# Performance work log

Measured on AMD Instinct MI355X. Metric: run time of the kernel, lower is better.

## Reference

```python
import jax, jax.numpy as jnp
import numpy as np

B, L, C = 2048, 2048, 16
F = L // 2                 # num_freqs = 1024
H = 4 * F                  # multi_factor * num_freqs = 4096
P = int(len(np.unique(L // np.arange(1, F + 1))))  # n patch sizes = 88
SCALE = 0.02
NOISE_EPS = 0.01


def setup_inputs() -> dict:
    key = jax.random.key(0)
    ks = jax.random.split(key, 10)
    return {
        "x": jax.random.normal(ks[0], (B, L, C), jnp.float32),
        "w_start": SCALE * jax.random.normal(ks[1], (C, 1), jnp.float32),
        "b_start": SCALE * jax.random.normal(ks[2], (1,), jnp.float32),
        "w1": SCALE * jax.random.normal(ks[3], (2, F, H), jnp.float32),
        "b1": SCALE * jax.random.normal(ks[4], (2, H), jnp.float32),
        "w2": SCALE * jax.random.normal(ks[5], (2, H, F), jnp.float32),
        "b2": SCALE * jax.random.normal(ks[6], (2, F), jnp.float32),
        "w_gate": SCALE * jax.random.normal(ks[7], (F, P), jnp.float32),
        "w_noise": SCALE * jax.random.normal(ks[8], (F, P), jnp.float32),
        "noise_z": jax.random.normal(ks[9], (B, P), jnp.float32),
        "top_k": 3,
    }


def reference(x, w_start, b_start, w1, b1, w2, b2, w_gate, w_noise, noise_z, top_k):
    # start_fc: [B, L, C] -> [B, L, 1] -> [B, 1, L]
    v = (jnp.einsum("blc,co->blo", x, w_start) + b_start).transpose(0, 2, 1)
    # rfft (ortho), drop DC bin -> [B, 1, F] complex
    xf = jnp.fft.rfft(v, axis=-1, norm="ortho")[:, :, 1:]
    xr, xi = jnp.real(xf), jnp.imag(xf)
    # complex 2-layer MLP in frequency domain
    o1r = jax.nn.relu(jnp.einsum("bdi,io->bdo", xr, w1[0]) - jnp.einsum("bdi,io->bdo", xi, w1[1]) + b1[0])
    o1i = jax.nn.relu(jnp.einsum("bdi,io->bdo", xi, w1[0]) + jnp.einsum("bdi,io->bdo", xr, w1[1]) + b1[1])
    o2r = jnp.einsum("bdo,of->bdf", o1r, w2[0]) - jnp.einsum("bdo,of->bdf", o1i, w2[1]) + b2[0]
    o2i = jnp.einsum("bdo,of->bdf", o1i, w2[0]) + jnp.einsum("bdo,of->bdf", o1r, w2[1]) + b2[1]
    amp = jnp.sqrt(o2r * o2r + o2i * o2i)[:, 0, :]  # [B, F]
    # router logits with (training) noise injection
    clean_logits = amp @ w_gate                      # [B, P]
    noise_std = jax.nn.softplus(amp @ w_noise) + NOISE_EPS
    logits = clean_logits + noise_z * noise_std
    # top-k -> softmax over top-k -> scatter into sparse gates
    top_w, top_i = jax.lax.top_k(logits, top_k)
    top_w = jax.nn.softmax(top_w, axis=-1)
    rows = jnp.arange(logits.shape[0])[:, None]
    gates = jnp.zeros_like(logits).at[rows, top_i].set(top_w)
    return gates
```

## Files before the change

kernel.cpp:

```cpp
#include <hip/hip_runtime.h>
#include <hip/hip_bf16.h>
#include <math.h>

#define B_DIM 2048
#define L_DIM 2048
#define F_DIM 1024
#define H_DIM 4096
#define P_DIM 88

typedef unsigned short u16;
typedef short bf16x8 __attribute__((ext_vector_type(8)));
typedef float f32x4 __attribute__((ext_vector_type(4)));

__device__ __forceinline__ u16 f2bf(float x) {
    unsigned u = __float_as_uint(x);
    return (u16)((u + 0x7fffu + ((u >> 16) & 1u)) >> 16);
}
__device__ __forceinline__ float bf2f(u16 h) {
    return __uint_as_float(((unsigned)h) << 16);
}

__device__ __forceinline__ void gload_lds16(const void* g, void* l) {
    unsigned loff = (unsigned)(uintptr_t)l;
    __builtin_amdgcn_global_load_lds(
        reinterpret_cast<const __attribute__((address_space(1))) void*>(
            reinterpret_cast<uintptr_t>(g)),
        reinterpret_cast<__attribute__((address_space(3))) void*>(loff),
        16, 0, 0);
}

__global__ __launch_bounds__(256) void prep_kernel(
    const float* __restrict__ x, const float* __restrict__ w_start,
    const float* __restrict__ b_start, u16* __restrict__ A1,
    const float* __restrict__ w1, u16* __restrict__ BT1)
{
    __shared__ float re[2048];
    __shared__ float im[2048];
    __shared__ float twr[1024];
    __shared__ float twi[1024];
    __shared__ float t0s[32][33];
    __shared__ float t1s[32][33];

    const int tid = threadIdx.x;

    if (blockIdx.x < 1024) {
        int b = blockIdx.x;
        const size_t row0 = (size_t)(2 * b) * 2048;

        const float4* wp = (const float4*)w_start;
        float4 w0 = wp[0], w1v = wp[1], w2 = wp[2], w3 = wp[3];
        float bs = b_start[0];

        for (int i = tid; i < 1024; i += 256) {
            float ang = -6.283185307179586f * ((float)i / 2048.0f);
            sincosf(ang, &twi[i], &twr[i]);
        }

        for (int l = tid; l < 2048; l += 256) {
            const float4* xp0 = (const float4*)(x + (row0 + l) * 16);
            const float4* xp1 = (const float4*)(x + (row0 + 2048 + l) * 16);
            float4 a0 = xp0[0], a1 = xp0[1], a2 = xp0[2], a3 = xp0[3];
            float4 c0 = xp1[0], c1 = xp1[1], c2 = xp1[2], c3 = xp1[3];
            float va = bs, vb = bs;
            va += a0.x * w0.x + a0.y * w0.y + a0.z * w0.z + a0.w * w0.w;
            va += a1.x * w1v.x + a1.y * w1v.y + a1.z * w1v.z + a1.w * w1v.w;
            va += a2.x * w2.x + a2.y * w2.y + a2.z * w2.z + a2.w * w2.w;
            va += a3.x * w3.x + a3.y * w3.y + a3.z * w3.z + a3.w * w3.w;
            vb += c0.x * w0.x + c0.y * w0.y + c0.z * w0.z + c0.w * w0.w;
            vb += c1.x * w1v.x + c1.y * w1v.y + c1.z * w1v.z + c1.w * w1v.w;
            vb += c2.x * w2.x + c2.y * w2.y + c2.z * w2.z + c2.w * w2.w;
            vb += c3.x * w3.x + c3.y * w3.y + c3.z * w3.z + c3.w * w3.w;
            unsigned j = __brev((unsigned)l) >> 21;
            re[j] = va;
            im[j] = vb;
        }
        __syncthreads();

        for (int s = 1; s <= 11; s++) {
            int half = 1 << (s - 1);
            for (int t = tid; t < 1024; t += 256) {
                int j = t & (half - 1);
                int base = (t >> (s - 1)) << s;
                int idx = j << (11 - s);
                float wr = twr[idx], wi = twi[idx];
                int i0 = base + j, i1 = i0 + half;
                float br = re[i1], bi = im[i1];
                float tr = br * wr - bi * wi;
                float ti = br * wi + bi * wr;
                float ar = re[i0], ai = im[i0];
                re[i0] = ar + tr; im[i0] = ai + ti;
                re[i1] = ar - tr; im[i1] = ai - ti;
            }
            __syncthreads();
        }

        const float sc = 0.5f * 0.022097086912079612f;
        u16* r0 = A1 + (size_t)(2 * b) * 4096;
        u16* r1 = r0 + 4096;
        for (int t = tid; t < 1024; t += 256) {
            int k = t + 1;
            int nk = 2048 - k;
            float Zr = re[k], Zi = im[k], Yr = re[nk], Yi = im[nk];
            float Ar = (Zr + Yr) * sc;
            float Ai = (Zi - Yi) * sc;
            float Br = (Zi + Yi) * sc;
            float Bi = (Yr - Zr) * sc;
            u16 h, lo;
            h = f2bf(Ar); lo = f2bf(Ar - bf2f(h)); r0[t] = h; r0[1024 + t] = lo;
            h = f2bf(Ai); lo = f2bf(Ai - bf2f(h)); r0[2048 + t] = h; r0[3072 + t] = lo;
            h = f2bf(Br); lo = f2bf(Br - bf2f(h)); r1[t] = h; r1[1024 + t] = lo;
            h = f2bf(Bi); lo = f2bf(Bi - bf2f(h)); r1[2048 + t] = h; r1[3072 + t] = lo;
        }
    } else {
        const int Kc = F_DIM, Nh = H_DIM;
        int bid = blockIdx.x - 1024;
        int k0 = (bid & 31) * 32;
        int n0 = (bid >> 5) * 32;
        int tx = tid & 31, ty = tid >> 5;
        const float* w0 = w1;
        const float* w1b = w1 + (size_t)Kc * Nh;

#pragma unroll
        for (int i = 0; i < 4; i++) {
            int k = k0 + ty + 8 * i;
            t0s[ty + 8 * i][tx] = w0[(size_t)k * Nh + n0 + tx];
            t1s[ty + 8 * i][tx] = w1b[(size_t)k * Nh + n0 + tx];
        }
        __syncthreads();

        size_t K4 = 4 * (size_t)Kc;
        int k = k0 + tx;
#pragma unroll
        for (int i = 0; i < 4; i++) {
            int nl = ty + 8 * i;
            int n = n0 + nl;
            float br = t0s[tx][nl];
            float bi = t1s[tx][nl];
            u16 brh = f2bf(br); u16 brl = f2bf(br - bf2f(brh));
            float nbi = -bi;
            u16 nih = f2bf(nbi); u16 nil = f2bf(nbi - bf2f(nih));
            u16 pih = f2bf(bi);  u16 pil = f2bf(bi - bf2f(pih));
            u16* rowr = BT1 + (size_t)n * K4;
            rowr[0 * Kc + k] = brh; rowr[1 * Kc + k] = brl;
            rowr[2 * Kc + k] = nih; rowr[3 * Kc + k] = nil;
            u16* rowi = BT1 + (size_t)(Nh + n) * K4;
            rowi[0 * Kc + k] = pih; rowi[1 * Kc + k] = pil;
            rowi[2 * Kc + k] = brh; rowi[3 * Kc + k] = brl;
        }
    }
}

__global__ __launch_bounds__(256) void conv_bt_kernel(
    const float* __restrict__ w, u16* __restrict__ BT, int Kc, int Nh)
{
    __shared__ float t0[32][33];
    __shared__ float t1[32][33];
    int k0 = blockIdx.x * 32, n0 = blockIdx.y * 32;
    int tx = threadIdx.x, ty = threadIdx.y;
    const float* w0 = w;
    const float* w1 = w + (size_t)Kc * Nh;

#pragma unroll
    for (int i = 0; i < 4; i++) {
        int k = k0 + ty + 8 * i;
        t0[ty + 8 * i][tx] = w0[(size_t)k * Nh + n0 + tx];
        t1[ty + 8 * i][tx] = w1[(size_t)k * Nh + n0 + tx];
    }
    __syncthreads();

    size_t K4 = 4 * (size_t)Kc;
    int k = k0 + tx;
#pragma unroll
    for (int i = 0; i < 4; i++) {
        int nl = ty + 8 * i;
        int n = n0 + nl;
        float br = t0[tx][nl];
        float bi = t1[tx][nl];
        u16 brh = f2bf(br); u16 brl = f2bf(br - bf2f(brh));
        float nbi = -bi;
        u16 nih = f2bf(nbi); u16 nil = f2bf(nbi - bf2f(nih));
        u16 pih = f2bf(bi);  u16 pil = f2bf(bi - bf2f(pih));
        u16* rowr = BT + (size_t)n * K4;
        rowr[0 * Kc + k] = brh; rowr[1 * Kc + k] = brl;
        rowr[2 * Kc + k] = nih; rowr[3 * Kc + k] = nil;
        u16* rowi = BT + (size_t)(Nh + n) * K4;
        rowi[0 * Kc + k] = pih; rowi[1 * Kc + k] = pil;
        rowi[2 * Kc + k] = brh; rowi[3 * Kc + k] = brl;
    }
}

extern __shared__ char smem8p[];

#define MFMA16(ACC0, ACC1, ACC2, ACC3, A0, A1, A2, A3, B0, B1, B2, B3)           \
    ACC0[0] = __builtin_amdgcn_mfma_f32_16x16x32_bf16(A0, B0, ACC0[0], 0, 0, 0); \
    ACC0[1] = __builtin_amdgcn_mfma_f32_16x16x32_bf16(A0, B1, ACC0[1], 0, 0, 0); \
    ACC0[2] = __builtin_amdgcn_mfma_f32_16x16x32_bf16(A0, B2, ACC0[2], 0, 0, 0); \
    ACC0[3] = __builtin_amdgcn_mfma_f32_16x16x32_bf16(A0, B3, ACC0[3], 0, 0, 0); \
    ACC1[0] = __builtin_amdgcn_mfma_f32_16x16x32_bf16(A1, B0, ACC1[0], 0, 0, 0); \
    ACC1[1] = __builtin_amdgcn_mfma_f32_16x16x32_bf16(A1, B1, ACC1[1], 0, 0, 0); \
    ACC1[2] = __builtin_amdgcn_mfma_f32_16x16x32_bf16(A1, B2, ACC1[2], 0, 0, 0); \
    ACC1[3] = __builtin_amdgcn_mfma_f32_16x16x32_bf16(A1, B3, ACC1[3], 0, 0, 0); \
    ACC2[0] = __builtin_amdgcn_mfma_f32_16x16x32_bf16(A2, B0, ACC2[0], 0, 0, 0); \
    ACC2[1] = __builtin_amdgcn_mfma_f32_16x16x32_bf16(A2, B1, ACC2[1], 0, 0, 0); \
    ACC2[2] = __builtin_amdgcn_mfma_f32_16x16x32_bf16(A2, B2, ACC2[2], 0, 0, 0); \
    ACC2[3] = __builtin_amdgcn_mfma_f32_16x16x32_bf16(A2, B3, ACC2[3], 0, 0, 0); \
    ACC3[0] = __builtin_amdgcn_mfma_f32_16x16x32_bf16(A3, B0, ACC3[0], 0, 0, 0); \
    ACC3[1] = __builtin_amdgcn_mfma_f32_16x16x32_bf16(A3, B1, ACC3[1], 0, 0, 0); \
    ACC3[2] = __builtin_amdgcn_mfma_f32_16x16x32_bf16(A3, B2, ACC3[2], 0, 0, 0); \
    ACC3[3] = __builtin_amdgcn_mfma_f32_16x16x32_bf16(A3, B3, ACC3[3], 0, 0, 0);

template <int EPI, int SWZ>
__global__ __launch_bounds__(512, 2) void gemm8p(
    const u16* __restrict__ A, const u16* __restrict__ B,
    const float* __restrict__ biasL, const float* __restrict__ biasR,
    u16* __restrict__ OutU, float* __restrict__ P01, float* __restrict__ P23,
    int Kc, int KcLog, int NH, int nt)
{
    char* ldsA = smem8p;
    char* ldsB = smem8p + 65536;

    const int tid = threadIdx.x;
    const int w = tid >> 6, lane = tid & 63;
    const int wr = w >> 2, wc = w & 3;
    const int fr = lane & 15, kb = lane >> 4;

    int bx, by, z;
    if (SWZ == 1) {
        int b = blockIdx.x;
        int xcd = b & 7, idx = b >> 3;
        bx = 4 * xcd + (idx & 3);
        by = idx >> 2;
        z = 0;
    } else if (SWZ == 2) {
        int b = blockIdx.x;
        by = b & 7;
        int s = b >> 3;
        bx = s & 7;
        z = s >> 3;
    } else {
        bx = blockIdx.x; by = blockIdx.y; z = blockIdx.z;
    }
    const int n0 = bx * 256, m0 = by * 256;
    const size_t K4 = 4 * (size_t)Kc;

    const int srow = tid >> 2;
    const int lk8 = (((tid & 3) ^ ((tid >> 3) & 3))) * 8;
    const int wb = (tid >> 6) * 1024;

    const int laneOff = fr * 64 + ((kb ^ ((fr >> 1) & 3)) << 4);

    f32x4 acc[8][4];
#pragma unroll
    for (int i = 0; i < 8; i++)
#pragma unroll
        for (int j = 0; j < 4; j++)
            acc[i][j] = (f32x4){0.f, 0.f, 0.f, 0.f};

    const int t0 = z * nt, te = t0 + nt;

    auto colA = [&](int t) {
        int k0 = t << 5;
        int seg = k0 >> KcLog, kk = k0 & (Kc - 1);
        int r3 = seg >= 3 ? seg - 3 : seg;
        int bs = seg >= 3 ? 2 : 0;
        return (bs + (r3 == 1 ? 1 : 0)) * Kc + kk;
    };
    auto colB = [&](int t) {
        int k0 = t << 5;
        int seg = k0 >> KcLog, kk = k0 & (Kc - 1);
        int r3 = seg >= 3 ? seg - 3 : seg;
        int bs = seg >= 3 ? 2 : 0;
        return (bs + (r3 == 2 ? 1 : 0)) * Kc + kk;
    };
    auto stageA = [&](int t) {
        const u16* src = A + (size_t)(m0 + srow) * K4 + colA(t) + lk8;
        char* dst = ldsA + (t & 3) * 16384 + wb;
        gload_lds16(src, dst);
        gload_lds16(src + (size_t)128 * K4, dst + 8192);
    };
    auto stageB = [&](int t) {
        const u16* src = B + (size_t)(n0 + srow) * K4 + colB(t) + lk8;
        char* dst = ldsB + (t & 3) * 16384 + wb;
        gload_lds16(src, dst);
        gload_lds16(src + (size_t)128 * K4, dst + 8192);
    };
    auto aBase = [&](int t) -> const char* {
        return ldsA + (t & 3) * 16384 + wr * 8192 + laneOff;
    };
    auto bBase = [&](int t) -> const char* {
        return ldsB + (t & 3) * 16384 + wc * 4096 + laneOff;
    };

    stageA(t0); stageB(t0);
    if (t0 + 1 < te) { stageA(t0 + 1); stageB(t0 + 1); }
    if (t0 + 1 < te) asm volatile("s_waitcnt vmcnt(4)" ::: "memory");
    else             asm volatile("s_waitcnt vmcnt(0)" ::: "memory");
    asm volatile("s_barrier" ::: "memory");

    bf16x8 b0, b1, b2, b3, a0, a1, a2, a3;
    {
        const char* aS = aBase(t0);
        const char* bS = bBase(t0);
        b0 = *(const bf16x8*)(bS + 0 * 1024);
        b1 = *(const bf16x8*)(bS + 1 * 1024);
        b2 = *(const bf16x8*)(bS + 2 * 1024);
        b3 = *(const bf16x8*)(bS + 3 * 1024);
        a0 = *(const bf16x8*)(aS + 0 * 1024);
        a1 = *(const bf16x8*)(aS + 1 * 1024);
        a2 = *(const bf16x8*)(aS + 2 * 1024);
        a3 = *(const bf16x8*)(aS + 3 * 1024);
    }

    for (int t = t0; t < te; ++t) {
        const bool haveStage = (t + 2 < te);
        const bool haveNext  = (t + 1 < te);

        if (haveStage) { stageA(t + 2); stageB(t + 2); }

        const char* aS = aBase(t);
        bf16x8 c0 = *(const bf16x8*)(aS + 4096 + 0 * 1024);
        bf16x8 c1 = *(const bf16x8*)(aS + 4096 + 1 * 1024);
        bf16x8 c2 = *(const bf16x8*)(aS + 4096 + 2 * 1024);
        bf16x8 c3 = *(const bf16x8*)(aS + 4096 + 3 * 1024);

        __builtin_amdgcn_s_setprio(1);
        MFMA16(acc[0], acc[1], acc[2], acc[3], a0, a1, a2, a3, b0, b1, b2, b3)
        __builtin_amdgcn_s_setprio(0);

        if (haveStage) asm volatile("s_waitcnt vmcnt(4)" ::: "memory");
        else           asm volatile("s_waitcnt vmcnt(0)" ::: "memory");
        asm volatile("s_barrier" ::: "memory");

        if (haveNext) {
            const char* aN = aBase(t + 1);
            a0 = *(const bf16x8*)(aN + 0 * 1024);
            a1 = *(const bf16x8*)(aN + 1 * 1024);
            a2 = *(const bf16x8*)(aN + 2 * 1024);
            a3 = *(const bf16x8*)(aN + 3 * 1024);
        }

        __builtin_amdgcn_s_setprio(1);
        MFMA16(acc[4], acc[5], acc[6], acc[7], c0, c1, c2, c3, b0, b1, b2, b3)
        __builtin_amdgcn_s_setprio(0);

        if (haveNext) {
            const char* bN = bBase(t + 1);
            b0 = *(const bf16x8*)(bN + 0 * 1024);
            b1 = *(const bf16x8*)(bN + 1 * 1024);
            b2 = *(const bf16x8*)(bN + 2 * 1024);
            b3 = *(const bf16x8*)(bN + 3 * 1024);
        }
    }

    const int fq = kb;
#pragma unroll
    for (int nj = 0; nj < 4; nj++) {
        int n = n0 + wc * 64 + nj * 16 + fr;
        if (EPI == 0) {
            bool left = (n < NH);
            int nn = left ? n : (n - NH);
            float bias = left ? biasL[n] : biasR[nn];
#pragma unroll
            for (int mi = 0; mi < 8; mi++) {
                int mb = m0 + wr * 128 + mi * 16 + fq * 4;
#pragma unroll
                for (int r = 0; r < 4; r++) {
                    float val = fmaxf(acc[mi][nj][r] + bias, 0.f);
                    u16 h = f2bf(val);
                    u16 lo = f2bf(val - bf2f(h));
                    size_t rb = (size_t)(mb + r) * (4 * (size_t)NH);
                    if (left) { OutU[rb + nn] = h; OutU[rb + NH + nn] = lo; }
                    else { OutU[rb + 2 * (size_t)NH + nn] = h; OutU[rb + 3 * (size_t)NH + nn] = lo; }
                }
            }
        } else {
            const size_t PSZ = (size_t)2048 * 2048;
            float* Out = (z < 2) ? (P01 + (size_t)z * PSZ) : (P23 + (size_t)(z - 2) * PSZ);
#pragma unroll
            for (int mi = 0; mi < 8; mi++) {
                int mb = m0 + wr * 128 + mi * 16 + fq * 4;
#pragma unroll
                for (int r = 0; r < 4; r++)
                    Out[(size_t)(mb + r) * 2048 + n] = acc[mi][nj][r];
            }
        }
    }
}

__global__ __launch_bounds__(256) void router_kernel(
    const float* __restrict__ P01, const float* __restrict__ P23, int ZK,
    const float* __restrict__ b2,
    const float* __restrict__ w_gate, const float* __restrict__ w_noise,
    const float* __restrict__ noise_z, float* __restrict__ gates)
{
    __shared__ float s_amp[8][1024];
    __shared__ float s_dot[8][176];
    __shared__ float s_lg[8][88];
    __shared__ int   s_idx[8][3];
    __shared__ float s_val[8][3];

    const int tid = threadIdx.x;
    const int r0 = blockIdx.x * 8;
    const size_t PSZ = (size_t)2048 * 2048;

    for (int idx = tid; idx < 8 * 1024; idx += 256) {
        int row = idx >> 10, i = idx & 1023;
        size_t roff = (size_t)(r0 + row) * 2048;
        float orr = b2[i];
        float oii = b2[1024 + i];
        for (int zz = 0; zz < ZK; zz++) {
            const float* Pz = ((zz < 2) ? (P01 + (size_t)zz * PSZ)
                                        : (P23 + (size_t)(zz - 2) * PSZ)) + roff;
            orr += Pz[i];
            oii += Pz[1024 + i];
        }
        s_amp[row][i] = sqrtf(orr * orr + oii * oii);
    }
    __syncthreads();

    for (int idx = tid; idx < 8 * 176; idx += 256) {
        int row = idx / 176, c = idx % 176;
        const float* wcol = (c < 88) ? (w_gate + c) : (w_noise + (c - 88));
        float s = 0.f;
        const float4* av = (const float4*)s_amp[row];
        for (int k4 = 0; k4 < 256; k4++) {
            float4 a = av[k4];
            int k = k4 * 4;
            s = fmaf(a.x, wcol[(size_t)(k + 0) * 88], s);
            s = fmaf(a.y, wcol[(size_t)(k + 1) * 88], s);
            s = fmaf(a.z, wcol[(size_t)(k + 2) * 88], s);
            s = fmaf(a.w, wcol[(size_t)(k + 3) * 88], s);
        }
        s_dot[row][c] = s;
    }
    __syncthreads();

    for (int idx = tid; idx < 8 * 88; idx += 256) {
        int row = idx / 88, c = idx % 88;
        float cn = s_dot[row][88 + c];
        float ns = (cn > 20.f) ? cn : log1pf(expf(cn));
        ns += 0.01f;
        s_lg[row][c] = s_dot[row][c] + noise_z[(size_t)(r0 + row) * 88 + c] * ns;
    }
    __syncthreads();

    if (tid < 8) {
        int i0 = -1, i1 = -1, i2 = -1;
        float v0 = -1e30f, v1 = -1e30f, v2 = -1e30f;
        for (int i = 0; i < P_DIM; i++) {
            float t = s_lg[tid][i];
            if (t > v0) { v0 = t; i0 = i; }
        }
        for (int i = 0; i < P_DIM; i++) {
            if (i == i0) continue;
            float t = s_lg[tid][i];
            if (t > v1) { v1 = t; i1 = i; }
        }
        for (int i = 0; i < P_DIM; i++) {
            if (i == i0 || i == i1) continue;
            float t = s_lg[tid][i];
            if (t > v2) { v2 = t; i2 = i; }
        }
        s_idx[tid][0] = i0; s_idx[tid][1] = i1; s_idx[tid][2] = i2;
        s_val[tid][0] = v0; s_val[tid][1] = v1; s_val[tid][2] = v2;
    }
    __syncthreads();

    for (int idx = tid; idx < 8 * 88; idx += 256) {
        int row = idx / 88, c = idx % 88;
        float m = s_val[row][0];
        float e0 = expf(s_val[row][0] - m);
        float e1 = expf(s_val[row][1] - m);
        float e2 = expf(s_val[row][2] - m);
        float inv = 1.f / (e0 + e1 + e2);
        float g = 0.f;
        if (c == s_idx[row][0]) g = e0 * inv;
        else if (c == s_idx[row][1]) g = e1 * inv;
        else if (c == s_idx[row][2]) g = e2 * inv;
        gates[(size_t)(r0 + row) * 88 + c] = g;
    }
}

extern "C" void kernel_launch(void* const* d_in, const int* in_sizes, int n_in,
                              void* d_out, int out_size, void* d_ws, size_t ws_size,
                              hipStream_t stream)
{
    const float* x       = (const float*)d_in[0];
    const float* w_start = (const float*)d_in[1];
    const float* b_start = (const float*)d_in[2];
    const float* w1      = (const float*)d_in[3];
    const float* b1      = (const float*)d_in[4];
    const float* w2      = (const float*)d_in[5];
    const float* b2      = (const float*)d_in[6];
    const float* w_gate  = (const float*)d_in[7];
    const float* w_noise = (const float*)d_in[8];
    const float* noise_z = (const float*)d_in[9];
    float* gates = (float*)d_out;

    const size_t MB = 1024 * 1024;
    char* base = (char*)d_ws;
    u16*  A1   = (u16*)(base + 16 * MB);
    u16*  BT   = (u16*)(base + 32 * MB);
    u16*  A2   = (u16*)(base + 96 * MB);
    float* P01 = (float*)base;
    float* P23 = (float*)(base + 160 * MB);

    int ZK = (ws_size >= (size_t)192 * MB) ? 4 : 2;

    hipFuncSetAttribute(reinterpret_cast<const void*>(&gemm8p<0, 1>),
                        hipFuncAttributeMaxDynamicSharedMemorySize, 131072);
    hipFuncSetAttribute(reinterpret_cast<const void*>(&gemm8p<1, 2>),
                        hipFuncAttributeMaxDynamicSharedMemorySize, 131072);

    prep_kernel<<<1024 + 4096, 256, 0, stream>>>(
        x, w_start, b_start, A1, w1, BT);

    gemm8p<0, 1><<<256, 512, 131072, stream>>>(
        A1, BT, b1, b1 + H_DIM, A2, nullptr, nullptr, F_DIM, 10, H_DIM, 192);

    conv_bt_kernel<<<dim3(H_DIM / 32, F_DIM / 32), dim3(32, 8), 0, stream>>>(
        w2, BT, H_DIM, F_DIM);
    gemm8p<1, 2><<<64 * ZK, 512, 131072, stream>>>(
        A2, BT, nullptr, nullptr, nullptr, P01, P23, H_DIM, 12, F_DIM, 768 / ZK);

    router_kernel<<<B_DIM / 8, 256, 0, stream>>>(
        P01, P23, ZK, b2, w_gate, w_noise, noise_z, gates);
}
```

Before: 583.5 us.

## Double GEMM block to 1024 threads with 4x4 warp grid

Changes the 256x256 tile GEMM from 8 waves (2x4) with 128x64 per wave to 16 waves (4x4) with 64x64 per wave. Each thread now issues one global->LDS load per stage instead of two, and the accumulator count is halved. This cuts per-thread register pressure and adds more waves to hide latency. In exchange, per-wave data reuse is lower and more LDS reads are issued per MFMA. Launch bounds of (1024,4) may be unrealistic with 128KB LDS per block.

```diff
diff --git a/kernel.cpp b/kernel.cpp
--- a/kernel.cpp
+++ b/kernel.cpp
@@ -191,26 +191,8 @@
 
 extern __shared__ char smem8p[];
 
-#define MFMA16(ACC0, ACC1, ACC2, ACC3, A0, A1, A2, A3, B0, B1, B2, B3)           \
-    ACC0[0] = __builtin_amdgcn_mfma_f32_16x16x32_bf16(A0, B0, ACC0[0], 0, 0, 0); \
-    ACC0[1] = __builtin_amdgcn_mfma_f32_16x16x32_bf16(A0, B1, ACC0[1], 0, 0, 0); \
-    ACC0[2] = __builtin_amdgcn_mfma_f32_16x16x32_bf16(A0, B2, ACC0[2], 0, 0, 0); \
-    ACC0[3] = __builtin_amdgcn_mfma_f32_16x16x32_bf16(A0, B3, ACC0[3], 0, 0, 0); \
-    ACC1[0] = __builtin_amdgcn_mfma_f32_16x16x32_bf16(A1, B0, ACC1[0], 0, 0, 0); \
-    ACC1[1] = __builtin_amdgcn_mfma_f32_16x16x32_bf16(A1, B1, ACC1[1], 0, 0, 0); \
-    ACC1[2] = __builtin_amdgcn_mfma_f32_16x16x32_bf16(A1, B2, ACC1[2], 0, 0, 0); \
-    ACC1[3] = __builtin_amdgcn_mfma_f32_16x16x32_bf16(A1, B3, ACC1[3], 0, 0, 0); \
-    ACC2[0] = __builtin_amdgcn_mfma_f32_16x16x32_bf16(A2, B0, ACC2[0], 0, 0, 0); \
-    ACC2[1] = __builtin_amdgcn_mfma_f32_16x16x32_bf16(A2, B1, ACC2[1], 0, 0, 0); \
-    ACC2[2] = __builtin_amdgcn_mfma_f32_16x16x32_bf16(A2, B2, ACC2[2], 0, 0, 0); \
-    ACC2[3] = __builtin_amdgcn_mfma_f32_16x16x32_bf16(A2, B3, ACC2[3], 0, 0, 0); \
-    ACC3[0] = __builtin_amdgcn_mfma_f32_16x16x32_bf16(A3, B0, ACC3[0], 0, 0, 0); \
-    ACC3[1] = __builtin_amdgcn_mfma_f32_16x16x32_bf16(A3, B1, ACC3[1], 0, 0, 0); \
-    ACC3[2] = __builtin_amdgcn_mfma_f32_16x16x32_bf16(A3, B2, ACC3[2], 0, 0, 0); \
-    ACC3[3] = __builtin_amdgcn_mfma_f32_16x16x32_bf16(A3, B3, ACC3[3], 0, 0, 0);
-
 template <int EPI, int SWZ>
-__global__ __launch_bounds__(512, 2) void gemm8p(
+__global__ __launch_bounds__(1024, 4) void gemm8p(
     const u16* __restrict__ A, const u16* __restrict__ B,
     const float* __restrict__ biasL, const float* __restrict__ biasR,
     u16* __restrict__ OutU, float* __restrict__ P01, float* __restrict__ P23,
@@ -245,13 +227,13 @@
 
     const int srow = tid >> 2;
     const int lk8 = (((tid & 3) ^ ((tid >> 3) & 3))) * 8;
-    const int wb = (tid >> 6) * 1024;
+    const int wb = w * 1024;
 
     const int laneOff = fr * 64 + ((kb ^ ((fr >> 1) & 3)) << 4);
 
-    f32x4 acc[8][4];
-#pragma unroll
-    for (int i = 0; i < 8; i++)
+    f32x4 acc[4][4];
+#pragma unroll
+    for (int i = 0; i < 4; i++)
 #pragma unroll
         for (int j = 0; j < 4; j++)
             acc[i][j] = (f32x4){0.f, 0.f, 0.f, 0.f};
@@ -274,41 +256,38 @@
     };
     auto stageA = [&](int t) {
         const u16* src = A + (size_t)(m0 + srow) * K4 + colA(t) + lk8;
-        char* dst = ldsA + (t & 3) * 16384 + wb;
-        gload_lds16(src, dst);
-        gload_lds16(src + (size_t)128 * K4, dst + 8192);
+        gload_lds16(src, ldsA + (t & 3) * 16384 + wb);
     };
     auto stageB = [&](int t) {
         const u16* src = B + (size_t)(n0 + srow) * K4 + colB(t) + lk8;
-        char* dst = ldsB + (t & 3) * 16384 + wb;
-        gload_lds16(src, dst);
-        gload_lds16(src + (size_t)128 * K4, dst + 8192);
+        gload_lds16(src, ldsB + (t & 3) * 16384 + wb);
     };
     auto aBase = [&](int t) -> const char* {
-        return ldsA + (t & 3) * 16384 + wr * 8192 + laneOff;
+        return ldsA + (t & 3) * 16384 + wr * 4096 + laneOff;
     };
     auto bBase = [&](int t) -> const char* {
         return ldsB + (t & 3) * 16384 + wc * 4096 + laneOff;
     };
 
     stageA(t0); stageB(t0);
-    if (t0 + 1 < te) { stageA(t0 + 1); stageB(t0 + 1); }
-    if (t0 + 1 < te) asm volatile("s_waitcnt vmcnt(4)" ::: "memory");
-    else             asm volatile("s_waitcnt vmcnt(0)" ::: "memory");
+    if (t0 + 1 < te) {
+        stageA(t0 + 1); stageB(t0 + 1);
+        asm volatile("s_waitcnt vmcnt(2)" ::: "memory");
+    } else {
+        asm volatile("s_waitcnt vmcnt(0)" ::: "memory");
+    }
     asm volatile("s_barrier" ::: "memory");
 
-    bf16x8 b0, b1, b2, b3, a0, a1, a2, a3;
+    bf16x8 a0, a1, b0, b1, b2, b3;
     {
         const char* aS = aBase(t0);
         const char* bS = bBase(t0);
+        a0 = *(const bf16x8*)(aS + 0 * 1024);
+        a1 = *(const bf16x8*)(aS + 1 * 1024);
         b0 = *(const bf16x8*)(bS + 0 * 1024);
         b1 = *(const bf16x8*)(bS + 1 * 1024);
         b2 = *(const bf16x8*)(bS + 2 * 1024);
         b3 = *(const bf16x8*)(bS + 3 * 1024);
-        a0 = *(const bf16x8*)(aS + 0 * 1024);
-        a1 = *(const bf16x8*)(aS + 1 * 1024);
-        a2 = *(const bf16x8*)(aS + 2 * 1024);
-        a3 = *(const bf16x8*)(aS + 3 * 1024);
     }
 
     for (int t = t0; t < te; ++t) {
@@ -318,16 +297,21 @@
         if (haveStage) { stageA(t + 2); stageB(t + 2); }
 
         const char* aS = aBase(t);
-        bf16x8 c0 = *(const bf16x8*)(aS + 4096 + 0 * 1024);
-        bf16x8 c1 = *(const bf16x8*)(aS + 4096 + 1 * 1024);
-        bf16x8 c2 = *(const bf16x8*)(aS + 4096 + 2 * 1024);
-        bf16x8 c3 = *(const bf16x8*)(aS + 4096 + 3 * 1024);
+        bf16x8 c0 = *(const bf16x8*)(aS + 2 * 1024);
+        bf16x8 c1 = *(const bf16x8*)(aS + 3 * 1024);
 
         __builtin_amdgcn_s_setprio(1);
-        MFMA16(acc[0], acc[1], acc[2], acc[3], a0, a1, a2, a3, b0, b1, b2, b3)
+        acc[0][0] = __builtin_amdgcn_mfma_f32_16x16x32_bf16(a0, b0, acc[0][0], 0, 0, 0);
+        acc[0][1] = __builtin_amdgcn_mfma_f32_16x16x32_bf16(a0, b1, acc[0][1], 0, 0, 0);
+        acc[0][2] = __builtin_amdgcn_mfma_f32_16x16x32_bf16(a0, b2, acc[0][2], 0, 0, 0);
+        acc[0][3] = __builtin_amdgcn_mfma_f32_16x16x32_bf16(a0, b3, acc[0][3], 0, 0, 0);
+        acc[1][0] = __builtin_amdgcn_mfma_f32_16x16x32_bf16(a1, b0, acc[1][0], 0, 0, 0);
+        acc[1][1] = __builtin_amdgcn_mfma_f32_16x16x32_bf16(a1, b1, acc[1][1], 0, 0, 0);
+        acc[1][2] = __builtin_amdgcn_mfma_f32_16x16x32_bf16(a1, b2, acc[1][2], 0, 0, 0);
+        acc[1][3] = __builtin_amdgcn_mfma_f32_16x16x32_bf16(a1, b3, acc[1][3], 0, 0, 0);
         __builtin_amdgcn_s_setprio(0);
 
-        if (haveStage) asm volatile("s_waitcnt vmcnt(4)" ::: "memory");
+        if (haveStage) asm volatile("s_waitcnt vmcnt(2)" ::: "memory");
         else           asm volatile("s_waitcnt vmcnt(0)" ::: "memory");
         asm volatile("s_barrier" ::: "memory");
 
@@ -335,12 +319,17 @@
             const char* aN = aBase(t + 1);
             a0 = *(const bf16x8*)(aN + 0 * 1024);
             a1 = *(const bf16x8*)(aN + 1 * 1024);
-            a2 = *(const bf16x8*)(aN + 2 * 1024);
-            a3 = *(const bf16x8*)(aN + 3 * 1024);
         }
 
         __builtin_amdgcn_s_setprio(1);
-        MFMA16(acc[4], acc[5], acc[6], acc[7], c0, c1, c2, c3, b0, b1, b2, b3)
+        acc[2][0] = __builtin_amdgcn_mfma_f32_16x16x32_bf16(c0, b0, acc[2][0], 0, 0, 0);
+        acc[2][1] = __builtin_amdgcn_mfma_f32_16x16x32_bf16(c0, b1, acc[2][1], 0, 0, 0);
+        acc[2][2] = __builtin_amdgcn_mfma_f32_16x16x32_bf16(c0, b2, acc[2][2], 0, 0, 0);
+        acc[2][3] = __builtin_amdgcn_mfma_f32_16x16x32_bf16(c0, b3, acc[2][3], 0, 0, 0);
+        acc[3][0] = __builtin_amdgcn_mfma_f32_16x16x32_bf16(c1, b0, acc[3][0], 0, 0, 0);
+        acc[3][1] = __builtin_amdgcn_mfma_f32_16x16x32_bf16(c1, b1, acc[3][1], 0, 0, 0);
+        acc[3][2] = __builtin_amdgcn_mfma_f32_16x16x32_bf16(c1, b2, acc[3][2], 0, 0, 0);
+        acc[3][3] = __builtin_amdgcn_mfma_f32_16x16x32_bf16(c1, b3, acc[3][3], 0, 0, 0);
         __builtin_amdgcn_s_setprio(0);
 
         if (haveNext) {
@@ -361,8 +350,8 @@
             int nn = left ? n : (n - NH);
             float bias = left ? biasL[n] : biasR[nn];
 #pragma unroll
-            for (int mi = 0; mi < 8; mi++) {
-                int mb = m0 + wr * 128 + mi * 16 + fq * 4;
+            for (int mi = 0; mi < 4; mi++) {
+                int mb = m0 + wr * 64 + mi * 16 + fq * 4;
 #pragma unroll
                 for (int r = 0; r < 4; r++) {
                     float val = fmaxf(acc[mi][nj][r] + bias, 0.f);
@@ -377,8 +366,8 @@
             const size_t PSZ = (size_t)2048 * 2048;
             float* Out = (z < 2) ? (P01 + (size_t)z * PSZ) : (P23 + (size_t)(z - 2) * PSZ);
 #pragma unroll
-            for (int mi = 0; mi < 8; mi++) {
-                int mb = m0 + wr * 128 + mi * 16 + fq * 4;
+            for (int mi = 0; mi < 4; mi++) {
+                int mb = m0 + wr * 64 + mi * 16 + fq * 4;
 #pragma unroll
                 for (int r = 0; r < 4; r++)
                     Out[(size_t)(mb + r) * 2048 + n] = acc[mi][nj][r];
@@ -515,12 +504,12 @@
     prep_kernel<<<1024 + 4096, 256, 0, stream>>>(
         x, w_start, b_start, A1, w1, BT);
 
-    gemm8p<0, 1><<<256, 512, 131072, stream>>>(
+    gemm8p<0, 1><<<256, 1024, 131072, stream>>>(
         A1, BT, b1, b1 + H_DIM, A2, nullptr, nullptr, F_DIM, 10, H_DIM, 192);
 
     conv_bt_kernel<<<dim3(H_DIM / 32, F_DIM / 32), dim3(32, 8), 0, stream>>>(
         w2, BT, H_DIM, F_DIM);
-    gemm8p<1, 2><<<64 * ZK, 512, 131072, stream>>>(
+    gemm8p<1, 2><<<64 * ZK, 1024, 131072, stream>>>(
         A2, BT, nullptr, nullptr, nullptr, P01, P23, H_DIM, 12, F_DIM, 768 / ZK);
 
     router_kernel<<<B_DIM / 8, 256, 0, stream>>>(
```

After: 585.3 us. No clear change (+0.3%).
